# Kernel tuning notes

Measured on AMD Instinct MI355X. Metric: run time of the kernel, lower is better.

## Reference

```python
import jax, jax.numpy as jnp
import numpy as np

N_SPK, N_UTT, D = 512, 64, 1024
EPS = 1e-6  # matches tf.math.l2_normalize default epsilon guard


def _l2norm(x, axis=-1):
    return x / jnp.sqrt(jnp.maximum(jnp.sum(x * x, axis=axis, keepdims=True), EPS))


def setup_inputs() -> dict:
    key = jax.random.key(0)
    k1, _ = jax.random.split(key)
    inputs = jax.random.normal(k1, (N_SPK, N_UTT, D), dtype=jnp.float32)
    w = jnp.asarray(10.0, dtype=jnp.float32)
    b = jnp.asarray(-5.0, dtype=jnp.float32)
    return {"inputs": inputs, "w": w, "b": b}


def reference(inputs, w, b):
    N, M, _ = inputs.shape
    # speaker centroids: mean over utterances -> [N, D]
    centroids = jnp.mean(inputs, axis=1)
    # utterance (exclusion) centroids: mean of the other M-1 utterances -> [N, M, D]
    ut_centroids = (jnp.sum(inputs, axis=1, keepdims=True) - inputs) / (M - 1)

    e = _l2norm(inputs)          # [N, M, D]
    c = _l2norm(centroids)       # [N, D]
    uc = _l2norm(ut_centroids)   # [N, M, D]

    # cosine sim of every utterance vs every speaker centroid -> [N, M, K]
    cos_all = jnp.einsum('nmd,kd->nmk', e, c)
    # same-speaker entries use the self-exclusion centroid
    cos_self = jnp.sum(e * uc, axis=-1)  # [N, M]
    eye = jnp.eye(N, dtype=inputs.dtype)[:, None, :]  # [N, 1, N]
    cos_sim = cos_all * (1.0 - eye) + cos_self[:, :, None] * eye

    sim = w * cos_sim + b  # [N, M, N]
    # softmax contrastive loss: -S_{j,i,j} + logsumexp_k S_{j,i,k}, summed
    lse = jax.nn.logsumexp(sim, axis=-1)            # [N, M]
    pos = jnp.einsum('nmn->nm', sim)                # diagonal along speaker axes
    loss = jnp.sum(lse - pos)
    return loss
```

## Files before the change

kernel.cpp:

```cpp
#include <hip/hip_runtime.h>
#include <stdint.h>

#define N_SPK 512
#define N_UTT 64
#define DIM   1024
#define NROWS (N_SPK * N_UTT)
#define EPS   1e-6f

#define BMF 128
#define BNF 512
#define BKF 32
#define KTF (DIM / BKF)
#define SLOT_BYTES 40960

typedef __attribute__((ext_vector_type(8))) short short8;
typedef __attribute__((ext_vector_type(4))) float f32x4;

__device__ __forceinline__ uint16_t f2bf(float f) {
    union { float f; uint32_t i; } un; un.f = f;
    uint32_t x = un.i;
    return (uint16_t)((x + 0x7fffu + ((x >> 16) & 1u)) >> 16);
}

__global__ __launch_bounds__(256) void prep_centroid(
    const float* __restrict__ x, uint16_t* __restrict__ xb,
    uint16_t* __restrict__ cmat, float* __restrict__ xxg,
    float* __restrict__ ssqg)
{
    const int n    = blockIdx.x;
    const int tid  = threadIdx.x;
    const int lane = tid & 63;
    const int w    = tid >> 6;

    const float* xn  = x  + (size_t)n * N_UTT * DIM;
    uint16_t*    xbn = xb + (size_t)n * N_UTT * DIM;

    float Sp[16];
    #pragma unroll
    for (int j = 0; j < 16; ++j) Sp[j] = 0.f;

    #pragma unroll 1
    for (int o = 0; o < 4; ++o) {
        const int m0 = w * 16 + o * 4;

        float4 v[16];
        #pragma unroll
        for (int i = 0; i < 4; ++i)
            #pragma unroll
            for (int j = 0; j < 4; ++j)
                v[i * 4 + j] = *(const float4*)(xn + (size_t)(m0 + i) * DIM + j * 256 + lane * 4);

        float xx[4] = {0.f, 0.f, 0.f, 0.f};
        #pragma unroll
        for (int i = 0; i < 4; ++i) {
            #pragma unroll
            for (int j = 0; j < 4; ++j) {
                const float4 qv = v[i * 4 + j];
                xx[i] += qv.x * qv.x + qv.y * qv.y + qv.z * qv.z + qv.w * qv.w;
                Sp[j * 4 + 0] += qv.x; Sp[j * 4 + 1] += qv.y;
                Sp[j * 4 + 2] += qv.z; Sp[j * 4 + 3] += qv.w;
                ushort4 ov;
                ov.x = f2bf(qv.x); ov.y = f2bf(qv.y); ov.z = f2bf(qv.z); ov.w = f2bf(qv.w);
                *(ushort4*)(xbn + (size_t)(m0 + i) * DIM + j * 256 + lane * 4) = ov;
            }
        }

        #pragma unroll
        for (int i = 0; i < 4; ++i) {
            float t = xx[i];
            #pragma unroll
            for (int off = 1; off < 64; off <<= 1) t += __shfl_xor(t, off);
            if (lane == 0) xxg[n * N_UTT + m0 + i] = t;
        }
    }

    __shared__ float Sh[4][DIM];
    #pragma unroll
    for (int j = 0; j < 4; ++j)
        *(float4*)&Sh[w][j * 256 + lane * 4] =
            make_float4(Sp[j * 4], Sp[j * 4 + 1], Sp[j * 4 + 2], Sp[j * 4 + 3]);
    __syncthreads();

    const int d0 = tid * 4;
    float4 S  = *(const float4*)&Sh[0][d0];
    const float4 b1 = *(const float4*)&Sh[1][d0];
    const float4 b2 = *(const float4*)&Sh[2][d0];
    const float4 b3 = *(const float4*)&Sh[3][d0];
    S.x += b1.x + b2.x + b3.x; S.y += b1.y + b2.y + b3.y;
    S.z += b1.z + b2.z + b3.z; S.w += b1.w + b2.w + b3.w;

    float css = S.x * S.x + S.y * S.y + S.z * S.z + S.w * S.w;
    #pragma unroll
    for (int off = 1; off < 64; off <<= 1) css += __shfl_xor(css, off);
    __shared__ float red[4];
    if ((tid & 63) == 0) red[tid >> 6] = css;
    __syncthreads();
    const float ssq = red[0] + red[1] + red[2] + red[3];

    const float scale = rsqrtf(fmaxf(ssq * (1.0f / 4096.f), EPS)) * (1.0f / 64.f);
    ushort4 oc;
    oc.x = f2bf(S.x * scale); oc.y = f2bf(S.y * scale);
    oc.z = f2bf(S.z * scale); oc.w = f2bf(S.w * scale);
    *(ushort4*)(cmat + (size_t)n * DIM + d0) = oc;
    if (tid == 0) ssqg[n] = ssq;
}

__global__ __launch_bounds__(512, 1) void gemm_lse_kernel(
    const uint16_t* __restrict__ xb, const uint16_t* __restrict__ cmat,
    const float* __restrict__ xxg, const float* __restrict__ ssqg,
    const float* __restrict__ wp, const float* __restrict__ bp,
    float* __restrict__ partial)
{
    __shared__ char smem[3 * SLOT_BYTES];

    const int tid   = threadIdx.x;
    const int lane  = tid & 63;
    const int wid   = tid >> 6;
    const int waveM = wid >> 2;
    const int waveN = wid & 3;

    const int rowBase = blockIdx.x * BMF;

    const uint16_t* gsrc[5];
    int ldso[5];
    {
        const int srow = tid >> 2;
        const int kc   = (tid & 3) ^ ((srow >> 1) & 3);
        gsrc[0] = xb + (size_t)(rowBase + srow) * DIM + kc * 8;
        ldso[0] = tid * 16;
    }
    #pragma unroll
    for (int i = 1; i < 5; ++i) {
        const int s    = tid + (i - 1) * 512;
        const int brow = s >> 2;
        const int kc   = (s & 3) ^ ((brow >> 1) & 3);
        gsrc[i] = cmat + (size_t)brow * DIM + kc * 8;
        ldso[i] = 8192 + s * 16;
    }

#define STAGE(slot, kt_)                                                        \
    { _Pragma("unroll")                                                         \
      for (int i_ = 0; i_ < 5; ++i_) {                                          \
        __builtin_amdgcn_global_load_lds(                                       \
            (const __attribute__((address_space(1))) void*)(gsrc[i_] + (kt_) * BKF), \
            (__attribute__((address_space(3))) void*)(smem + (slot) * SLOT_BYTES + ldso[i_]), \
            16, 0, 0); } }

    f32x4 acc[4][8];
    #pragma unroll
    for (int i = 0; i < 4; ++i)
        #pragma unroll
        for (int j = 0; j < 8; ++j)
            acc[i][j] = (f32x4){0.f, 0.f, 0.f, 0.f};

    const int cL  = lane & 15;
    const int q   = lane >> 4;
    const int kcs = q ^ ((cL >> 1) & 3);

#define COMPUTE(slot_)                                                          \
    {                                                                           \
        const char* Ab_ = smem + (slot_) * SLOT_BYTES;                          \
        const char* Bb_ = smem + (slot_) * SLOT_BYTES + 8192;                   \
        short8 a_[4], b_[8];                                                    \
        _Pragma("unroll")                                                       \
        for (int bi_ = 0; bi_ < 4; ++bi_)                                       \
            a_[bi_] = *(const short8*)(Ab_ + (waveM * 64 + bi_ * 16 + cL) * 64 + kcs * 16); \
        _Pragma("unroll")                                                       \
        for (int bj_ = 0; bj_ < 8; ++bj_)                                       \
            b_[bj_] = *(const short8*)(Bb_ + (waveN * 128 + bj_ * 16 + cL) * 64 + kcs * 16); \
        __builtin_amdgcn_s_setprio(1);                                          \
        _Pragma("unroll")                                                       \
        for (int bi_ = 0; bi_ < 4; ++bi_)                                       \
            _Pragma("unroll")                                                   \
            for (int bj_ = 0; bj_ < 8; ++bj_)                                   \
                acc[bi_][bj_] = __builtin_amdgcn_mfma_f32_16x16x32_bf16(        \
                    a_[bi_], b_[bj_], acc[bi_][bj_], 0, 0, 0);                  \
        __builtin_amdgcn_s_setprio(0);                                          \
    }

#define ITER(kt_, cSlot, sSlot)                                                 \
    {                                                                           \
        asm volatile("s_waitcnt vmcnt(5)" ::: "memory");                        \
        __builtin_amdgcn_sched_barrier(0);                                      \
        __builtin_amdgcn_s_barrier();                                           \
        __builtin_amdgcn_sched_barrier(0);                                      \
        STAGE(sSlot, (kt_) + 2);                                                \
        COMPUTE(cSlot);                                                         \
    }

    STAGE(0, 0);
    STAGE(1, 1);

    for (int tb = 0; tb < 30; tb += 3) {
        ITER(tb + 0, 0, 2);
        ITER(tb + 1, 1, 0);
        ITER(tb + 2, 2, 1);
    }
    asm volatile("s_waitcnt vmcnt(5)" ::: "memory");
    __builtin_amdgcn_sched_barrier(0);
    __builtin_amdgcn_s_barrier();
    __builtin_amdgcn_sched_barrier(0);
    COMPUTE(0);
    asm volatile("s_waitcnt vmcnt(0)" ::: "memory");
    __builtin_amdgcn_sched_barrier(0);
    __builtin_amdgcn_s_barrier();
    __builtin_amdgcn_sched_barrier(0);
    COMPUTE(1);
#undef STAGE
#undef COMPUTE
#undef ITER

    __syncthreads();
    float* Se  = (float*)smem;
    float* Pe  = (float*)(smem + 2048);
    float* red = (float*)(smem + 2560);

    const float wv = wp[0], bv = bp[0];
    #pragma unroll
    for (int bi = 0; bi < 4; ++bi) {
        #pragma unroll
        for (int r = 0; r < 4; ++r) {
            const int lr    = waveM * 64 + bi * 16 + q * 4 + r;
            const int R     = rowBase + lr;
            const float xxv = xxg[R];
            const float rn  = rsqrtf(fmaxf(xxv, EPS));
            const int nrow  = R >> 6;
            float s = 0.f;
            #pragma unroll
            for (int bj = 0; bj < 8; ++bj) {
                const int col = waveN * 128 + bj * 16 + cL;
                const float dot = acc[bi][bj][r];
                float sim;
                if (col == nrow) {
                    const float ssqv = ssqg[nrow];
                    const float xs   = dot * sqrtf(ssqv);
                    const float d2   = ssqv - 2.f * xs + xxv;
                    const float cs   = ((xs - xxv) * (1.f / 63.f)) * rn *
                                       rsqrtf(fmaxf(d2 * (1.f / 3969.f), EPS));
                    sim = wv * cs + bv;
                    Pe[lr] = sim;
                } else {
                    sim = wv * (dot * rn) + bv;
                }
                s += __expf(sim);
            }
            #pragma unroll
            for (int off = 1; off < 16; off <<= 1) s += __shfl_xor(s, off);
            if (cL == 0) Se[waveN * 128 + lr] = s;
        }
    }
    __syncthreads();
    if (tid < 128) {
        const float tot = Se[tid] + Se[128 + tid] + Se[256 + tid] + Se[384 + tid];
        float lt = __logf(tot) - Pe[tid];
        #pragma unroll
        for (int off = 1; off < 64; off <<= 1) lt += __shfl_xor(lt, off);
        if ((tid & 63) == 0) red[tid >> 6] = lt;
    }
    __syncthreads();
    if (tid == 0) partial[blockIdx.x] = red[0] + red[1];
}

__global__ __launch_bounds__(256) void finalize_sum(
    const float* __restrict__ partial, float* __restrict__ out)
{
    const int tid = threadIdx.x;
    float t = partial[tid];
    #pragma unroll
    for (int off = 1; off < 64; off <<= 1) t += __shfl_xor(t, off);
    __shared__ float red[4];
    if ((tid & 63) == 0) red[tid >> 6] = t;
    __syncthreads();
    if (tid == 0) out[0] = red[0] + red[1] + red[2] + red[3];
}

extern "C" void kernel_launch(void* const* d_in, const int* in_sizes, int n_in,
                              void* d_out, int out_size, void* d_ws, size_t ws_size,
                              hipStream_t stream)
{
    const float* x  = (const float*)d_in[0];
    const float* wp = (const float*)d_in[1];
    const float* bp = (const float*)d_in[2];
    float* out = (float*)d_out;

    char* ws = (char*)d_ws;
    size_t off = 0;
    uint16_t* xb      = (uint16_t*)(ws + off); off += (size_t)NROWS * DIM * 2;
    uint16_t* cmat    = (uint16_t*)(ws + off); off += (size_t)N_SPK * DIM * 2;
    float*    xxg     = (float*)(ws + off);    off += (size_t)NROWS * 4;
    float*    ssqg    = (float*)(ws + off);    off += (size_t)N_SPK * 4;
    float*    partial = (float*)(ws + off);    off += (size_t)256 * 4;

    prep_centroid<<<N_SPK, 256, 0, stream>>>(x, xb, cmat, xxg, ssqg);
    gemm_lse_kernel<<<NROWS / BMF, 512, 0, stream>>>(
        xb, cmat, xxg, ssqg, wp, bp, partial);
    finalize_sum<<<1, 256, 0, stream>>>(partial, out);
}
```

Measured before the change: 244.2 us.

## Fuse bf16 conversion of utterance rows into GEMM A-tile loading

The prep kernel no longer writes a bf16 copy of all utterance embeddings. The GEMM kernel now reads fp32 rows directly into registers, converts them to bf16, and writes them into the LDS pipeline slot after the MFMA compute. This removes a 64 MB intermediate write and the separate bf16 buffer. In exchange the GEMM reads twice as many bytes for A and takes on register pressure and an extra register round trip in its pipeline.

```diff
diff --git a/kernel.cpp b/kernel.cpp
--- a/kernel.cpp
+++ b/kernel.cpp
@@ -23,7 +23,7 @@
 }
 
 __global__ __launch_bounds__(256) void prep_centroid(
-    const float* __restrict__ x, uint16_t* __restrict__ xb,
+    const float* __restrict__ x,
     uint16_t* __restrict__ cmat, float* __restrict__ xxg,
     float* __restrict__ ssqg)
 {
@@ -32,8 +32,7 @@
     const int lane = tid & 63;
     const int w    = tid >> 6;
 
-    const float* xn  = x  + (size_t)n * N_UTT * DIM;
-    uint16_t*    xbn = xb + (size_t)n * N_UTT * DIM;
+    const float* xn = x + (size_t)n * N_UTT * DIM;
 
     float Sp[16];
     #pragma unroll
@@ -59,9 +58,6 @@
                 xx[i] += qv.x * qv.x + qv.y * qv.y + qv.z * qv.z + qv.w * qv.w;
                 Sp[j * 4 + 0] += qv.x; Sp[j * 4 + 1] += qv.y;
                 Sp[j * 4 + 2] += qv.z; Sp[j * 4 + 3] += qv.w;
-                ushort4 ov;
-                ov.x = f2bf(qv.x); ov.y = f2bf(qv.y); ov.z = f2bf(qv.z); ov.w = f2bf(qv.w);
-                *(ushort4*)(xbn + (size_t)(m0 + i) * DIM + j * 256 + lane * 4) = ov;
             }
         }
 
@@ -106,7 +102,7 @@
 }
 
 __global__ __launch_bounds__(512, 1) void gemm_lse_kernel(
-    const uint16_t* __restrict__ xb, const uint16_t* __restrict__ cmat,
+    const float* __restrict__ x, const uint16_t* __restrict__ cmat,
     const float* __restrict__ xxg, const float* __restrict__ ssqg,
     const float* __restrict__ wp, const float* __restrict__ bp,
     float* __restrict__ partial)
@@ -121,30 +117,42 @@
 
     const int rowBase = blockIdx.x * BMF;
 
-    const uint16_t* gsrc[5];
-    int ldso[5];
+    const float* gAx;
     {
         const int srow = tid >> 2;
         const int kc   = (tid & 3) ^ ((srow >> 1) & 3);
-        gsrc[0] = xb + (size_t)(rowBase + srow) * DIM + kc * 8;
-        ldso[0] = tid * 16;
-    }
-    #pragma unroll
-    for (int i = 1; i < 5; ++i) {
-        const int s    = tid + (i - 1) * 512;
+        gAx = x + (size_t)(rowBase + srow) * DIM + kc * 8;
+    }
+    const uint16_t* gB[4];
+    int ldsoB[4];
+    #pragma unroll
+    for (int i = 0; i < 4; ++i) {
+        const int s    = tid + i * 512;
         const int brow = s >> 2;
         const int kc   = (s & 3) ^ ((brow >> 1) & 3);
-        gsrc[i] = cmat + (size_t)brow * DIM + kc * 8;
-        ldso[i] = 8192 + s * 16;
-    }
-
-#define STAGE(slot, kt_)                                                        \
+        gB[i]   = cmat + (size_t)brow * DIM + kc * 8;
+        ldsoB[i] = 8192 + s * 16;
+    }
+
+#define STAGE_B(slot, kt_)                                                      \
     { _Pragma("unroll")                                                         \
-      for (int i_ = 0; i_ < 5; ++i_) {                                          \
+      for (int i_ = 0; i_ < 4; ++i_) {                                          \
         __builtin_amdgcn_global_load_lds(                                       \
-            (const __attribute__((address_space(1))) void*)(gsrc[i_] + (kt_) * BKF), \
-            (__attribute__((address_space(3))) void*)(smem + (slot) * SLOT_BYTES + ldso[i_]), \
+            (const __attribute__((address_space(1))) void*)(gB[i_] + (kt_) * BKF), \
+            (__attribute__((address_space(3))) void*)(smem + (slot) * SLOT_BYTES + ldsoB[i_]), \
             16, 0, 0); } }
+
+#define LOAD_A(kt_, va, vb)                                                     \
+    { va = *(const float4*)(gAx + (kt_) * BKF);                                 \
+      vb = *(const float4*)(gAx + (kt_) * BKF + 4); }
+
+#define PACK_WRITE_A(slot, va, vb)                                              \
+    { union { uint32_t u[4]; short8 s8; } pk_;                                  \
+      pk_.u[0] = (uint32_t)f2bf(va.x) | ((uint32_t)f2bf(va.y) << 16);           \
+      pk_.u[1] = (uint32_t)f2bf(va.z) | ((uint32_t)f2bf(va.w) << 16);           \
+      pk_.u[2] = (uint32_t)f2bf(vb.x) | ((uint32_t)f2bf(vb.y) << 16);           \
+      pk_.u[3] = (uint32_t)f2bf(vb.z) | ((uint32_t)f2bf(vb.w) << 16);           \
+      *(short8*)(smem + (slot) * SLOT_BYTES + tid * 16) = pk_.s8; }
 
     f32x4 acc[4][8];
     #pragma unroll
@@ -180,23 +188,31 @@
 
 #define ITER(kt_, cSlot, sSlot)                                                 \
     {                                                                           \
-        asm volatile("s_waitcnt vmcnt(5)" ::: "memory");                        \
+        asm volatile("s_waitcnt vmcnt(4)" ::: "memory");                        \
         __builtin_amdgcn_sched_barrier(0);                                      \
         __builtin_amdgcn_s_barrier();                                           \
         __builtin_amdgcn_sched_barrier(0);                                      \
-        STAGE(sSlot, (kt_) + 2);                                                \
+        float4 va_, vb_;                                                        \
+        LOAD_A((kt_) + 2, va_, vb_);                                            \
+        STAGE_B(sSlot, (kt_) + 2);                                              \
         COMPUTE(cSlot);                                                         \
-    }
-
-    STAGE(0, 0);
-    STAGE(1, 1);
+        __builtin_amdgcn_sched_barrier(0);                                      \
+        PACK_WRITE_A(sSlot, va_, vb_);                                          \
+    }
+
+    {
+        float4 va, vb;
+        LOAD_A(0, va, vb); STAGE_B(0, 0); PACK_WRITE_A(0, va, vb);
+        LOAD_A(1, va, vb); STAGE_B(1, 1); PACK_WRITE_A(1, va, vb);
+    }
+    asm volatile("s_waitcnt lgkmcnt(0)" ::: "memory");
 
     for (int tb = 0; tb < 30; tb += 3) {
         ITER(tb + 0, 0, 2);
         ITER(tb + 1, 1, 0);
         ITER(tb + 2, 2, 1);
     }
-    asm volatile("s_waitcnt vmcnt(5)" ::: "memory");
+    asm volatile("s_waitcnt vmcnt(4)" ::: "memory");
     __builtin_amdgcn_sched_barrier(0);
     __builtin_amdgcn_s_barrier();
     __builtin_amdgcn_sched_barrier(0);
@@ -206,7 +222,9 @@
     __builtin_amdgcn_s_barrier();
     __builtin_amdgcn_sched_barrier(0);
     COMPUTE(1);
-#undef STAGE
+#undef STAGE_B
+#undef LOAD_A
+#undef PACK_WRITE_A
 #undef COMPUTE
 #undef ITER
 
@@ -285,14 +303,13 @@
 
     char* ws = (char*)d_ws;
     size_t off = 0;
-    uint16_t* xb      = (uint16_t*)(ws + off); off += (size_t)NROWS * DIM * 2;
     uint16_t* cmat    = (uint16_t*)(ws + off); off += (size_t)N_SPK * DIM * 2;
     float*    xxg     = (float*)(ws + off);    off += (size_t)NROWS * 4;
     float*    ssqg    = (float*)(ws + off);    off += (size_t)N_SPK * 4;
     float*    partial = (float*)(ws + off);    off += (size_t)256 * 4;
 
-    prep_centroid<<<N_SPK, 256, 0, stream>>>(x, xb, cmat, xxg, ssqg);
+    prep_centroid<<<N_SPK, 256, 0, stream>>>(x, cmat, xxg, ssqg);
     gemm_lse_kernel<<<NROWS / BMF, 512, 0, stream>>>(
-        xb, cmat, xxg, ssqg, wp, bp, partial);
+        x, cmat, xxg, ssqg, wp, bp, partial);
     finalize_sum<<<1, 256, 0, stream>>>(partial, out);
 }
```

Measured after the change: 246.0 us. No clear change (+0.7%).

## Halve GEMM row tile to 64, double-buffer, and raise occupancy

Applied to the files above, without the earlier changes.

Shrinks the fused GEMM+logsumexp row tile from 128 to 64 rows, which doubles the grid to 512 blocks. The triple-buffered LDS pipeline becomes double-buffered with a full vmcnt(0) wait, and launch bounds allow several blocks per CU. The aim is to fill all CUs (256 blocks under-fills a 256-CU part with one block each) and to hide latency through occupancy instead of prefetch depth. In exchange, each block re-streams the whole 512x1024 centroid matrix for half as many rows, so B-operand traffic doubles and arithmetic intensity per tile drops.

```diff
diff --git a/kernel.cpp b/kernel.cpp
--- a/kernel.cpp
+++ b/kernel.cpp
@@ -7,11 +7,10 @@
 #define NROWS (N_SPK * N_UTT)
 #define EPS   1e-6f
 
-#define BMF 128
-#define BNF 512
+#define BMF 64
 #define BKF 32
 #define KTF (DIM / BKF)
-#define SLOT_BYTES 40960
+#define SLOT_BYTES 36864
 
 typedef __attribute__((ext_vector_type(8))) short short8;
 typedef __attribute__((ext_vector_type(4))) float f32x4;
@@ -105,13 +104,13 @@
     if (tid == 0) ssqg[n] = ssq;
 }
 
-__global__ __launch_bounds__(512, 1) void gemm_lse_kernel(
+__global__ __launch_bounds__(512, 4) void gemm_lse_kernel(
     const uint16_t* __restrict__ xb, const uint16_t* __restrict__ cmat,
     const float* __restrict__ xxg, const float* __restrict__ ssqg,
     const float* __restrict__ wp, const float* __restrict__ bp,
     float* __restrict__ partial)
 {
-    __shared__ char smem[3 * SLOT_BYTES];
+    __shared__ char smem[2 * SLOT_BYTES];
 
     const int tid   = threadIdx.x;
     const int lane  = tid & 63;
@@ -121,34 +120,43 @@
 
     const int rowBase = blockIdx.x * BMF;
 
-    const uint16_t* gsrc[5];
-    int ldso[5];
-    {
+    const uint16_t* gA = nullptr;
+    int ldsoA = 0;
+    if (tid < 256) {
         const int srow = tid >> 2;
         const int kc   = (tid & 3) ^ ((srow >> 1) & 3);
-        gsrc[0] = xb + (size_t)(rowBase + srow) * DIM + kc * 8;
-        ldso[0] = tid * 16;
-    }
-    #pragma unroll
-    for (int i = 1; i < 5; ++i) {
-        const int s    = tid + (i - 1) * 512;
+        gA    = xb + (size_t)(rowBase + srow) * DIM + kc * 8;
+        ldsoA = tid * 16;
+    }
+    const uint16_t* gB[4];
+    int ldsoB[4];
+    #pragma unroll
+    for (int i = 0; i < 4; ++i) {
+        const int s    = tid + i * 512;
         const int brow = s >> 2;
         const int kc   = (s & 3) ^ ((brow >> 1) & 3);
-        gsrc[i] = cmat + (size_t)brow * DIM + kc * 8;
-        ldso[i] = 8192 + s * 16;
+        gB[i]    = cmat + (size_t)brow * DIM + kc * 8;
+        ldsoB[i] = 4096 + s * 16;
     }
 
 #define STAGE(slot, kt_)                                                        \
-    { _Pragma("unroll")                                                         \
-      for (int i_ = 0; i_ < 5; ++i_) {                                          \
-        __builtin_amdgcn_global_load_lds(                                       \
-            (const __attribute__((address_space(1))) void*)(gsrc[i_] + (kt_) * BKF), \
-            (__attribute__((address_space(3))) void*)(smem + (slot) * SLOT_BYTES + ldso[i_]), \
-            16, 0, 0); } }
-
-    f32x4 acc[4][8];
-    #pragma unroll
-    for (int i = 0; i < 4; ++i)
+    {                                                                           \
+        if (tid < 256)                                                          \
+            __builtin_amdgcn_global_load_lds(                                   \
+                (const __attribute__((address_space(1))) void*)(gA + (kt_) * BKF), \
+                (__attribute__((address_space(3))) void*)(smem + (slot) * SLOT_BYTES + ldsoA), \
+                16, 0, 0);                                                      \
+        _Pragma("unroll")                                                       \
+        for (int i_ = 0; i_ < 4; ++i_)                                          \
+            __builtin_amdgcn_global_load_lds(                                   \
+                (const __attribute__((address_space(1))) void*)(gB[i_] + (kt_) * BKF), \
+                (__attribute__((address_space(3))) void*)(smem + (slot) * SLOT_BYTES + ldsoB[i_]), \
+                16, 0, 0);                                                      \
+    }
+
+    f32x4 acc[2][8];
+    #pragma unroll
+    for (int i = 0; i < 2; ++i)
         #pragma unroll
         for (int j = 0; j < 8; ++j)
             acc[i][j] = (f32x4){0.f, 0.f, 0.f, 0.f};
@@ -160,17 +168,17 @@
 #define COMPUTE(slot_)                                                          \
     {                                                                           \
         const char* Ab_ = smem + (slot_) * SLOT_BYTES;                          \
-        const char* Bb_ = smem + (slot_) * SLOT_BYTES + 8192;                   \
-        short8 a_[4], b_[8];                                                    \
+        const char* Bb_ = smem + (slot_) * SLOT_BYTES + 4096;                   \
+        short8 a_[2], b_[8];                                                    \
         _Pragma("unroll")                                                       \
-        for (int bi_ = 0; bi_ < 4; ++bi_)                                       \
-            a_[bi_] = *(const short8*)(Ab_ + (waveM * 64 + bi_ * 16 + cL) * 64 + kcs * 16); \
+        for (int bi_ = 0; bi_ < 2; ++bi_)                                       \
+            a_[bi_] = *(const short8*)(Ab_ + (waveM * 32 + bi_ * 16 + cL) * 64 + kcs * 16); \
         _Pragma("unroll")                                                       \
         for (int bj_ = 0; bj_ < 8; ++bj_)                                       \
             b_[bj_] = *(const short8*)(Bb_ + (waveN * 128 + bj_ * 16 + cL) * 64 + kcs * 16); \
         __builtin_amdgcn_s_setprio(1);                                          \
         _Pragma("unroll")                                                       \
-        for (int bi_ = 0; bi_ < 4; ++bi_)                                       \
+        for (int bi_ = 0; bi_ < 2; ++bi_)                                       \
             _Pragma("unroll")                                                   \
             for (int bj_ = 0; bj_ < 8; ++bj_)                                   \
                 acc[bi_][bj_] = __builtin_amdgcn_mfma_f32_16x16x32_bf16(        \
@@ -180,26 +188,25 @@
 
 #define ITER(kt_, cSlot, sSlot)                                                 \
     {                                                                           \
-        asm volatile("s_waitcnt vmcnt(5)" ::: "memory");                        \
+        asm volatile("s_waitcnt vmcnt(0)" ::: "memory");                        \
         __builtin_amdgcn_sched_barrier(0);                                      \
         __builtin_amdgcn_s_barrier();                                           \
         __builtin_amdgcn_sched_barrier(0);                                      \
-        STAGE(sSlot, (kt_) + 2);                                                \
+        STAGE(sSlot, (kt_) + 1);                                                \
         COMPUTE(cSlot);                                                         \
     }
 
     STAGE(0, 0);
-    STAGE(1, 1);
-
-    for (int tb = 0; tb < 30; tb += 3) {
-        ITER(tb + 0, 0, 2);
+
+    for (int tb = 0; tb < 30; tb += 2) {
+        ITER(tb + 0, 0, 1);
         ITER(tb + 1, 1, 0);
-        ITER(tb + 2, 2, 1);
-    }
-    asm volatile("s_waitcnt vmcnt(5)" ::: "memory");
+    }
+    asm volatile("s_waitcnt vmcnt(0)" ::: "memory");
     __builtin_amdgcn_sched_barrier(0);
     __builtin_amdgcn_s_barrier();
     __builtin_amdgcn_sched_barrier(0);
+    STAGE(1, 31);
     COMPUTE(0);
     asm volatile("s_waitcnt vmcnt(0)" ::: "memory");
     __builtin_amdgcn_sched_barrier(0);
@@ -211,16 +218,15 @@
 #undef ITER
 
     __syncthreads();
-    float* Se  = (float*)smem;
-    float* Pe  = (float*)(smem + 2048);
-    float* red = (float*)(smem + 2560);
+    float* Se = (float*)smem;
+    float* Pe = (float*)(smem + 1024);
 
     const float wv = wp[0], bv = bp[0];
     #pragma unroll
-    for (int bi = 0; bi < 4; ++bi) {
+    for (int bi = 0; bi < 2; ++bi) {
         #pragma unroll
         for (int r = 0; r < 4; ++r) {
-            const int lr    = waveM * 64 + bi * 16 + q * 4 + r;
+            const int lr    = waveM * 32 + bi * 16 + q * 4 + r;
             const int R     = rowBase + lr;
             const float xxv = xxg[R];
             const float rn  = rsqrtf(fmaxf(xxv, EPS));
@@ -246,32 +252,35 @@
             }
             #pragma unroll
             for (int off = 1; off < 16; off <<= 1) s += __shfl_xor(s, off);
-            if (cL == 0) Se[waveN * 128 + lr] = s;
+            if (cL == 0) Se[waveN * 64 + lr] = s;
         }
     }
     __syncthreads();
-    if (tid < 128) {
-        const float tot = Se[tid] + Se[128 + tid] + Se[256 + tid] + Se[384 + tid];
+    if (tid < 64) {
+        const float tot = Se[tid] + Se[64 + tid] + Se[128 + tid] + Se[192 + tid];
         float lt = __logf(tot) - Pe[tid];
         #pragma unroll
         for (int off = 1; off < 64; off <<= 1) lt += __shfl_xor(lt, off);
-        if ((tid & 63) == 0) red[tid >> 6] = lt;
-    }
-    __syncthreads();
-    if (tid == 0) partial[blockIdx.x] = red[0] + red[1];
-}
-
-__global__ __launch_bounds__(256) void finalize_sum(
+        if (tid == 0) partial[blockIdx.x] = lt;
+    }
+}
+
+__global__ __launch_bounds__(512) void finalize_sum(
     const float* __restrict__ partial, float* __restrict__ out)
 {
     const int tid = threadIdx.x;
     float t = partial[tid];
     #pragma unroll
     for (int off = 1; off < 64; off <<= 1) t += __shfl_xor(t, off);
-    __shared__ float red[4];
+    __shared__ float red[8];
     if ((tid & 63) == 0) red[tid >> 6] = t;
     __syncthreads();
-    if (tid == 0) out[0] = red[0] + red[1] + red[2] + red[3];
+    if (tid == 0) {
+        float s = 0.f;
+        #pragma unroll
+        for (int i = 0; i < 8; ++i) s += red[i];
+        out[0] = s;
+    }
 }
 
 extern "C" void kernel_launch(void* const* d_in, const int* in_sizes, int n_in,
@@ -289,10 +298,10 @@
     uint16_t* cmat    = (uint16_t*)(ws + off); off += (size_t)N_SPK * DIM * 2;
     float*    xxg     = (float*)(ws + off);    off += (size_t)NROWS * 4;
     float*    ssqg    = (float*)(ws + off);    off += (size_t)N_SPK * 4;
-    float*    partial = (float*)(ws + off);    off += (size_t)256 * 4;
+    float*    partial = (float*)(ws + off);    off += (size_t)512 * 4;
 
     prep_centroid<<<N_SPK, 256, 0, stream>>>(x, xb, cmat, xxg, ssqg);
     gemm_lse_kernel<<<NROWS / BMF, 512, 0, stream>>>(
         xb, cmat, xxg, ssqg, wp, bp, partial);
-    finalize_sum<<<1, 256, 0, stream>>>(partial, out);
-}
+    finalize_sum<<<1, 512, 0, stream>>>(partial, out);
+}
```

After: 267.9 us. 9.7% more time.
